# Kernel optimization log

Hardware: AMD Instinct MI355X
Metric: run time of the kernel (lower is better)

## Reference

```python
import jax, jax.numpy as jnp
import numpy as np

NUM_HEADS = 16

def setup_inputs() -> dict:
    key = jax.random.key(0)
    k1, k2, k3 = jax.random.split(key, 3)
    T, B, E = 2048, 4, 1024
    x = jax.random.normal(k1, (T, B, E), dtype=jnp.float32)
    # xavier-ish scale for weights
    in_proj_w = jax.random.normal(k2, (3 * E, E), dtype=jnp.float32) * (1.0 / np.sqrt(E))
    in_proj_b = jnp.zeros((3 * E,), dtype=jnp.float32)
    out_w = jax.random.normal(k3, (E, E), dtype=jnp.float32) * (1.0 / np.sqrt(E))
    out_b = jnp.zeros((E,), dtype=jnp.float32)
    return {"x": x, "in_proj_w": in_proj_w, "in_proj_b": in_proj_b, "out_w": out_w, "out_b": out_b}

def reference(x, in_proj_w, in_proj_b, out_w, out_b):
    # Self-attention (qkv_same path), dropout=0, eval mode, no masks.
    T, B, E = x.shape
    H = NUM_HEADS
    Dh = E // H
    scaling = Dh ** (-0.5)
    # fused in-projection: [T,B,3E]
    qkv = jnp.einsum('tbe,fe->tbf', x, in_proj_w) + in_proj_b
    q, k, v = jnp.split(qkv, 3, axis=-1)
    q = q * scaling
    # [T,B,E] -> [B,H,T,Dh]
    def to_heads(t):
        return t.reshape(T, B, H, Dh).transpose(1, 2, 0, 3)
    q, k, v = to_heads(q), to_heads(k), to_heads(v)
    # full TxT score matrix, softmax in float32 (matches F.softmax(..., dtype=float32))
    scores = jnp.einsum('bhtd,bhsd->bhts', q, k)
    attn_weights = jax.nn.softmax(scores.astype(jnp.float32), axis=-1).astype(scores.dtype)
    attn = jnp.einsum('bhts,bhsd->bhtd', attn_weights, v)
    # [B,H,T,Dh] -> [T,B,E]
    attn = attn.transpose(2, 0, 1, 3).reshape(T, B, E)
    attn = jnp.einsum('tbe,fe->tbf', attn, out_w) + out_b
    # need_weights=True: average over heads -> [B,T,T]
    avg_weights = attn_weights.sum(axis=1) / H
    return attn, avg_weights
```

## Files before the change

kernel.cpp:

```cpp
#include <hip/hip_runtime.h>
#include <stdint.h>

#define DEV __device__ __forceinline__

typedef __attribute__((ext_vector_type(8))) __bf16 bf16x8;
typedef __attribute__((ext_vector_type(4))) __bf16 bf16x4;
typedef __attribute__((ext_vector_type(4))) float f32x4;

DEV unsigned short f2bf(float f){
  union { float fv; unsigned u; } v; v.fv = f;
  unsigned r = v.u + 0x7fffu + ((v.u >> 16) & 1u);
  return (unsigned short)(r >> 16);
}

DEV void gload16(const void* g, void* l){
  __builtin_amdgcn_global_load_lds((const __attribute__((address_space(1))) void*)g,
                                   (__attribute__((address_space(3))) void*)l,
                                   16, 0, 0);
}

__global__ void k_cvt(const float* __restrict__ src, unsigned short* __restrict__ dst){
  const int i = (blockIdx.x * blockDim.x + threadIdx.x) << 2;
  const float4 v = *(const float4*)(src + i);
  ushort4 o;
  o.x = f2bf(v.x); o.y = f2bf(v.y); o.z = f2bf(v.z); o.w = f2bf(v.w);
  *(ushort4*)(dst + i) = o;
}

template<int MODE>
__launch_bounds__(256)
__global__ void k_gemm(const unsigned short* __restrict__ A,
                       const unsigned short* __restrict__ Bm,
                       const float* __restrict__ bias,
                       float* __restrict__ outF,
                       unsigned short* __restrict__ Qm,
                       unsigned short* __restrict__ Km,
                       unsigned short* __restrict__ VTm)
{
  __shared__ unsigned short As[128*64];
  __shared__ unsigned short Bs[128*64];
  const int tid  = threadIdx.x;
  const int lane = tid & 63;
  const int wid  = tid >> 6;
  const int wr   = wid >> 1;
  const int wc   = wid & 1;
  const int wg = blockIdx.x;
  int bx, by;
  if (MODE == 0){ const int slot = wg >> 3; bx = (wg & 7) + 8*(slot >> 6); by = slot & 63; }
  else          { bx = wg & 7; by = wg >> 3; }
  const int r0   = by * 128;
  const int c0   = bx * 128;
  const int l15  = lane & 15;
  const int l4   = lane >> 4;

  f32x4 acc[4][4];
#pragma unroll
  for (int m = 0; m < 4; ++m)
#pragma unroll
    for (int n = 0; n < 4; ++n)
      acc[m][n] = (f32x4){0.f, 0.f, 0.f, 0.f};

  for (int k0 = 0; k0 < 1024; k0 += 64){
#pragma unroll
    for (int i = 0; i < 4; ++i){
      const int sb   = (i*4 + wid)*64;
      const int slot = sb + lane;
      const int row  = slot >> 3;
      const int cg   = (slot & 7) ^ (row & 7);
      gload16(A  + (size_t)(r0 + row)*1024 + k0 + cg*8, (void*)(As + sb*8));
      gload16(Bm + (size_t)(c0 + row)*1024 + k0 + cg*8, (void*)(Bs + sb*8));
    }
    __syncthreads();
#pragma unroll
    for (int kk = 0; kk < 2; ++kk){
      bf16x8 af[4], bf[4];
#pragma unroll
      for (int m = 0; m < 4; ++m){
        const int row = wr*64 + m*16 + l15;
        const int ch  = (kk*4 + l4) ^ (row & 7);
        af[m] = *(const bf16x8*)(As + row*64 + ch*8);
      }
#pragma unroll
      for (int n = 0; n < 4; ++n){
        const int row = wc*64 + n*16 + l15;
        const int ch  = (kk*4 + l4) ^ (row & 7);
        bf[n] = *(const bf16x8*)(Bs + row*64 + ch*8);
      }
#pragma unroll
      for (int m = 0; m < 4; ++m)
#pragma unroll
        for (int n = 0; n < 4; ++n)
          acc[m][n] = __builtin_amdgcn_mfma_f32_16x16x32_bf16(af[m], bf[n], acc[m][n], 0, 0, 0);
    }
    __syncthreads();
  }

  if (MODE == 0){
#pragma unroll
    for (int n = 0; n < 4; ++n){
      const int f     = c0 + wc*64 + n*16 + l15;
      const float bs  = bias[f];
      const int which = f >> 10;
      const int fi    = f & 1023;
      const int h     = fi >> 6;
      const int d     = fi & 63;
#pragma unroll
      for (int m = 0; m < 4; ++m){
        const int rb = r0 + wr*64 + m*16 + (l4 << 2);
#pragma unroll
        for (int j = 0; j < 4; ++j){
          const int r = rb + j;
          const int t = r >> 2;
          const int b = r & 3;
          float v = acc[m][n][j] + bs;
          if (which == 0) v *= 0.18033688f;
          const unsigned short bv = f2bf(v);
          const int bh = b*16 + h;
          if (which == 0)      Qm [((size_t)bh*2048 + t)*64 + d] = bv;
          else if (which == 1) Km [((size_t)bh*2048 + t)*64 + d] = bv;
          else                 VTm[((size_t)bh*64 + d)*2048 + t] = bv;
        }
      }
    }
  } else {
#pragma unroll
    for (int m = 0; m < 4; ++m){
      const int rb = r0 + wr*64 + m*16 + (l4 << 2);
#pragma unroll
      for (int n = 0; n < 4; ++n){
        const int f    = c0 + wc*64 + n*16 + l15;
        const float bs = bias[f];
#pragma unroll
        for (int j = 0; j < 4; ++j)
          outF[(size_t)(rb + j)*1024 + f] = acc[m][n][j] + bs;
      }
    }
  }
}

__launch_bounds__(512)
__global__ void k_pv(const unsigned short* __restrict__ Qm,
                     const unsigned short* __restrict__ Km,
                     const unsigned short* __restrict__ VTm,
                     float* __restrict__ linv,
                     unsigned short* __restrict__ ctx)
{
  __shared__ unsigned short Ws[256*64];
  __shared__ unsigned short Ks[2][64*64];
  __shared__ unsigned short Vs[2][64*64];
  const int tid = threadIdx.x, lane = tid & 63, wid = tid >> 6;
  const int l15 = lane & 15, l4 = lane >> 4;
  const int wg = blockIdx.x;
  const int slot = wg >> 3;
  const int bh = (wg & 7)*8 + (slot >> 3);
  const int t0 = (slot & 7) * 256;
  const unsigned short* Qb = Qm  + (size_t)bh*131072;
  const unsigned short* Kb = Km  + (size_t)bh*131072;
  const unsigned short* Vb = VTm + (size_t)bh*131072;

  {
    const int s = tid;
    const int row = s >> 3;
    const int cg = (s & 7) ^ (row & 7);
    gload16(Kb + (size_t)row*64 + cg*8, (void*)(Ks[0] + s*8));
    gload16(Vb + (size_t)row*2048 + cg*8, (void*)(Vs[0] + s*8));
  }
  bf16x8 aq[2][2];
#pragma unroll
  for (int qs = 0; qs < 2; ++qs)
#pragma unroll
    for (int kk = 0; kk < 2; ++kk)
      aq[qs][kk] = *(const bf16x8*)(Qb + (size_t)(t0 + wid*32 + qs*16 + l15)*64 + (kk*4 + l4)*8);
  __syncthreads();

  f32x4 oacc[2][4];
#pragma unroll
  for (int qs = 0; qs < 2; ++qs)
#pragma unroll
    for (int n = 0; n < 4; ++n) oacc[qs][n] = (f32x4){0.f,0.f,0.f,0.f};
  float lacc[2] = {0.f, 0.f};
  const int rx = l15 & 7;

  for (int s0 = 0; s0 < 2048; s0 += 64){
    const int cur = (s0 >> 6) & 1;
    if (s0 + 64 < 2048){
      const int s = tid;
      const int row = s >> 3;
      const int cg = (s & 7) ^ (row & 7);
      gload16(Kb + (size_t)(s0 + 64 + row)*64 + cg*8, (void*)(Ks[cur^1] + s*8));
      gload16(Vb + (size_t)row*2048 + (s0 + 64) + cg*8, (void*)(Vs[cur^1] + s*8));
    }
#pragma unroll
    for (int n = 0; n < 4; ++n){
      bf16x8 ak[2];
#pragma unroll
      for (int kk = 0; kk < 2; ++kk){
        const int ch = (kk*4 + l4) ^ rx;
        ak[kk] = *(const bf16x8*)(Ks[cur] + (n*16 + l15)*64 + ch*8);
      }
#pragma unroll
      for (int qs = 0; qs < 2; ++qs){
        f32x4 sacc = (f32x4){0.f,0.f,0.f,0.f};
        sacc = __builtin_amdgcn_mfma_f32_16x16x32_bf16(ak[0], aq[qs][0], sacc, 0, 0, 0);
        sacc = __builtin_amdgcn_mfma_f32_16x16x32_bf16(ak[1], aq[qs][1], sacc, 0, 0, 0);
        f32x4 pv;
        pv[0] = __builtin_amdgcn_exp2f(sacc[0]);
        pv[1] = __builtin_amdgcn_exp2f(sacc[1]);
        pv[2] = __builtin_amdgcn_exp2f(sacc[2]);
        pv[3] = __builtin_amdgcn_exp2f(sacc[3]);
        lacc[qs] += (pv[0] + pv[1]) + (pv[2] + pv[3]);
        const bf16x4 pb = __builtin_convertvector(pv, bf16x4);
        const int wrow = wid*32 + qs*16 + l15;
        const int g = (n*4 + l4) ^ (rx << 1);
        *(bf16x4*)(Ws + wrow*64 + g*4) = pb;
      }
    }
    bf16x8 aw[2][2];
#pragma unroll
    for (int qs = 0; qs < 2; ++qs)
#pragma unroll
      for (int kk = 0; kk < 2; ++kk){
        const int c = (kk*4 + l4) ^ rx;
        aw[qs][kk] = *(const bf16x8*)(Ws + (wid*32 + qs*16 + l15)*64 + c*8);
      }
#pragma unroll
    for (int n = 0; n < 4; ++n){
#pragma unroll
      for (int kk = 0; kk < 2; ++kk){
        const int ch = (kk*4 + l4) ^ rx;
        const bf16x8 bv = *(const bf16x8*)(Vs[cur] + (n*16 + l15)*64 + ch*8);
#pragma unroll
        for (int qs = 0; qs < 2; ++qs)
          oacc[qs][n] = __builtin_amdgcn_mfma_f32_16x16x32_bf16(aw[qs][kk], bv, oacc[qs][n], 0, 0, 0);
      }
    }
    __syncthreads();
  }

  const int b = bh >> 4, h = bh & 15;
#pragma unroll
  for (int qs = 0; qs < 2; ++qs){
    lacc[qs] += __shfl_xor(lacc[qs], 16);
    lacc[qs] += __shfl_xor(lacc[qs], 32);
    const float rl = 1.0f / lacc[qs];
    if (lane < 16)
      linv[(size_t)bh*2048 + t0 + wid*32 + qs*16 + lane] = rl;
    float rlj[4];
#pragma unroll
    for (int j = 0; j < 4; ++j)
      rlj[j] = __shfl(rl, (l4 << 2) + j);
#pragma unroll
    for (int n = 0; n < 4; ++n){
#pragma unroll
      for (int j = 0; j < 4; ++j){
        const int t = t0 + wid*32 + qs*16 + (l4 << 2) + j;
        const int d = n*16 + l15;
        ctx[((size_t)t*4 + b)*1024 + h*64 + d] = f2bf(oacc[qs][n][j] * rlj[j]);
      }
    }
  }
}

__launch_bounds__(256)
__global__ void k_avg(const unsigned short* __restrict__ Qm,
                      const unsigned short* __restrict__ Km,
                      const float* __restrict__ linv,
                      float* __restrict__ avg)
{
  __shared__ unsigned short Ks[2][128*64];
  const int tid = threadIdx.x, lane = tid & 63, wid = tid >> 6;
  const int l15 = lane & 15, l4 = lane >> 4;
  const int wg = blockIdx.x;
  const int slot = wg >> 3;
  const int combo = (wg & 7) + 8*(slot >> 4);
  const int b   = combo >> 4;
  const int s0  = (combo & 15) * 128;
  const int t0  = (slot & 15) * 128;
  const int rx  = l15 & 7;

  float wacc[2][8][4];
#pragma unroll
  for (int qs = 0; qs < 2; ++qs)
#pragma unroll
    for (int n = 0; n < 8; ++n)
#pragma unroll
      for (int j = 0; j < 4; ++j) wacc[qs][n][j] = 0.f;

  {
    const unsigned short* Kb = Km + (size_t)(b*16)*131072;
#pragma unroll
    for (int i = 0; i < 4; ++i){
      const int s = i*256 + tid;
      const int row = s >> 3;
      const int cg = (s & 7) ^ (row & 7);
      gload16(Kb + (size_t)(s0 + row)*64 + cg*8, (void*)(Ks[0] + s*8));
    }
  }
  __syncthreads();

  for (int h = 0; h < 16; ++h){
    const int cur = h & 1;
    if (h < 15){
      const unsigned short* Kb = Km + (size_t)(b*16 + h + 1)*131072;
#pragma unroll
      for (int i = 0; i < 4; ++i){
        const int s = i*256 + tid;
        const int row = s >> 3;
        const int cg = (s & 7) ^ (row & 7);
        gload16(Kb + (size_t)(s0 + row)*64 + cg*8, (void*)(Ks[cur^1] + s*8));
      }
    }
    const int bh = b*16 + h;
    const unsigned short* Qb = Qm + (size_t)bh*131072;

    bf16x8 aq[2][2];
#pragma unroll
    for (int qs = 0; qs < 2; ++qs)
#pragma unroll
      for (int kk = 0; kk < 2; ++kk)
        aq[qs][kk] = *(const bf16x8*)(Qb + (size_t)(t0 + wid*32 + qs*16 + l15)*64 + (kk*4 + l4)*8);

    float4 lj[2];
#pragma unroll
    for (int qs = 0; qs < 2; ++qs){
      lj[qs] = *(const float4*)(linv + (size_t)bh*2048 + t0 + wid*32 + qs*16 + (l4 << 2));
      lj[qs].x *= 0.0625f; lj[qs].y *= 0.0625f; lj[qs].z *= 0.0625f; lj[qs].w *= 0.0625f;
    }

#pragma unroll
    for (int n = 0; n < 8; ++n){
      bf16x8 bk[2];
#pragma unroll
      for (int kk = 0; kk < 2; ++kk){
        const int ch = (kk*4 + l4) ^ rx;
        bk[kk] = *(const bf16x8*)(Ks[cur] + (n*16 + l15)*64 + ch*8);
      }
#pragma unroll
      for (int qs = 0; qs < 2; ++qs){
        f32x4 sacc = (f32x4){0.f,0.f,0.f,0.f};
        sacc = __builtin_amdgcn_mfma_f32_16x16x32_bf16(aq[qs][0], bk[0], sacc, 0, 0, 0);
        sacc = __builtin_amdgcn_mfma_f32_16x16x32_bf16(aq[qs][1], bk[1], sacc, 0, 0, 0);
        wacc[qs][n][0] += __builtin_amdgcn_exp2f(sacc[0]) * lj[qs].x;
        wacc[qs][n][1] += __builtin_amdgcn_exp2f(sacc[1]) * lj[qs].y;
        wacc[qs][n][2] += __builtin_amdgcn_exp2f(sacc[2]) * lj[qs].z;
        wacc[qs][n][3] += __builtin_amdgcn_exp2f(sacc[3]) * lj[qs].w;
      }
    }
    __syncthreads();
  }

#pragma unroll
  for (int qs = 0; qs < 2; ++qs)
#pragma unroll
    for (int n = 0; n < 8; ++n)
#pragma unroll
      for (int j = 0; j < 4; ++j){
        const int t = t0 + wid*32 + qs*16 + (l4 << 2) + j;
        const int s = s0 + n*16 + l15;
        avg[((size_t)b*2048 + t)*2048 + s] = wacc[qs][n][j];
      }
}

extern "C" void kernel_launch(void* const* d_in, const int* in_sizes, int n_in,
                              void* d_out, int out_size, void* d_ws, size_t ws_size,
                              hipStream_t stream)
{
  const float* x    = (const float*)d_in[0];
  const float* wqkv = (const float*)d_in[1];
  const float* bqkv = (const float*)d_in[2];
  const float* wout = (const float*)d_in[3];
  const float* bout = (const float*)d_in[4];
  float* out = (float*)d_out;

  char* ws = (char*)d_ws;
  unsigned short* xb    = (unsigned short*)(ws);
  unsigned short* wqkvb = (unsigned short*)(ws + ((size_t)16 << 20));
  unsigned short* woutb = (unsigned short*)(ws + ((size_t)24 << 20));
  unsigned short* Qm    = (unsigned short*)(ws + ((size_t)26 << 20));
  unsigned short* Km    = (unsigned short*)(ws + ((size_t)42 << 20));
  unsigned short* VTm   = (unsigned short*)(ws + ((size_t)58 << 20));
  unsigned short* ctx   = (unsigned short*)(ws + ((size_t)74 << 20));
  float* linv = (float*)(ws + ((size_t)90 << 20));

  k_cvt<<<8192, 256, 0, stream>>>(x,    xb);
  k_cvt<<<3072, 256, 0, stream>>>(wqkv, wqkvb);
  k_cvt<<<1024, 256, 0, stream>>>(wout, woutb);

  k_gemm<0><<<1536, 256, 0, stream>>>(xb, wqkvb, bqkv, nullptr, Qm, Km, VTm);
  k_pv     <<< 512, 512, 0, stream>>>(Qm, Km, VTm, linv, ctx);
  k_avg    <<<1024, 256, 0, stream>>>(Qm, Km, linv, out + 8388608);
  k_gemm<1><<< 512, 256, 0, stream>>>(ctx, woutb, bout, out, nullptr, nullptr, nullptr);
}
```

Before: 287.4 us.

## Double-buffer GEMM LDS tiles with 128x256 tiles and 512-thread blocks

Rewrites the projection GEMM kernel to use 512-thread blocks computing 128x256 output tiles, with double-buffered LDS so the next K-slice loads while MFMAs run on the current one. Raw s_waitcnt/s_barrier replaces __syncthreads, and s_setprio raises priority around the MFMA bursts. Block-to-tile mapping is changed to group row tiles for L2 reuse. The larger LDS footprint (96KB) and launch_bounds(512,1) limit occupancy to one block per CU, and the hand-written vmcnt count must match the number of outstanding loads.

```diff
diff --git a/kernel.cpp b/kernel.cpp
--- a/kernel.cpp
+++ b/kernel.cpp
@@ -28,7 +28,7 @@
 }
 
 template<int MODE>
-__launch_bounds__(256)
+__launch_bounds__(512, 1)
 __global__ void k_gemm(const unsigned short* __restrict__ A,
                        const unsigned short* __restrict__ Bm,
                        const float* __restrict__ bias,
@@ -37,21 +37,20 @@
                        unsigned short* __restrict__ Km,
                        unsigned short* __restrict__ VTm)
 {
-  __shared__ unsigned short As[128*64];
-  __shared__ unsigned short Bs[128*64];
+  __shared__ unsigned short As[2][128*64];
+  __shared__ unsigned short Bs[2][256*64];
   const int tid  = threadIdx.x;
   const int lane = tid & 63;
   const int wid  = tid >> 6;
-  const int wr   = wid >> 1;
-  const int wc   = wid & 1;
-  const int wg = blockIdx.x;
-  int bx, by;
-  if (MODE == 0){ const int slot = wg >> 3; bx = (wg & 7) + 8*(slot >> 6); by = slot & 63; }
-  else          { bx = wg & 7; by = wg >> 3; }
-  const int r0   = by * 128;
-  const int c0   = bx * 128;
+  const int wr   = wid >> 2;
+  const int wc   = wid & 3;
   const int l15  = lane & 15;
   const int l4   = lane >> 4;
+  const int wg  = blockIdx.x;
+  const int by  = (wg & 7)*8 + ((wg >> 3) & 7);
+  const int bx  = wg >> 6;
+  const int r0  = by * 128;
+  const int c0  = bx * 256;
 
   f32x4 acc[4][4];
 #pragma unroll
@@ -60,17 +59,25 @@
     for (int n = 0; n < 4; ++n)
       acc[m][n] = (f32x4){0.f, 0.f, 0.f, 0.f};
 
-  for (int k0 = 0; k0 < 1024; k0 += 64){
+  auto STAGE = [&](int buf, int kt){
+    const int k0 = kt << 6;
+#pragma unroll
+    for (int i = 0; i < 2; ++i){
+      const int s = i*512 + tid;
+      const int row = s >> 3;
+      const int cg = (s & 7) ^ (row & 7);
+      gload16(A + (size_t)(r0 + row)*1024 + k0 + cg*8, (void*)(&As[buf][s*8]));
+    }
 #pragma unroll
     for (int i = 0; i < 4; ++i){
-      const int sb   = (i*4 + wid)*64;
-      const int slot = sb + lane;
-      const int row  = slot >> 3;
-      const int cg   = (slot & 7) ^ (row & 7);
-      gload16(A  + (size_t)(r0 + row)*1024 + k0 + cg*8, (void*)(As + sb*8));
-      gload16(Bm + (size_t)(c0 + row)*1024 + k0 + cg*8, (void*)(Bs + sb*8));
-    }
-    __syncthreads();
+      const int s = i*512 + tid;
+      const int row = s >> 3;
+      const int cg = (s & 7) ^ (row & 7);
+      gload16(Bm + (size_t)(c0 + row)*1024 + k0 + cg*8, (void*)(&Bs[buf][s*8]));
+    }
+  };
+
+  auto COMPUTE = [&](int buf){
 #pragma unroll
     for (int kk = 0; kk < 2; ++kk){
       bf16x8 af[4], bf[4];
@@ -78,22 +85,36 @@
       for (int m = 0; m < 4; ++m){
         const int row = wr*64 + m*16 + l15;
         const int ch  = (kk*4 + l4) ^ (row & 7);
-        af[m] = *(const bf16x8*)(As + row*64 + ch*8);
+        af[m] = *(const bf16x8*)(&As[buf][row*64 + ch*8]);
       }
 #pragma unroll
       for (int n = 0; n < 4; ++n){
         const int row = wc*64 + n*16 + l15;
         const int ch  = (kk*4 + l4) ^ (row & 7);
-        bf[n] = *(const bf16x8*)(Bs + row*64 + ch*8);
-      }
+        bf[n] = *(const bf16x8*)(&Bs[buf][row*64 + ch*8]);
+      }
+      __builtin_amdgcn_s_setprio(1);
 #pragma unroll
       for (int m = 0; m < 4; ++m)
 #pragma unroll
         for (int n = 0; n < 4; ++n)
           acc[m][n] = __builtin_amdgcn_mfma_f32_16x16x32_bf16(af[m], bf[n], acc[m][n], 0, 0, 0);
-    }
-    __syncthreads();
-  }
+      __builtin_amdgcn_s_setprio(0);
+    }
+  };
+
+  STAGE(0, 0);
+  for (int t = 0; t < 15; ++t){
+    const int cur = t & 1;
+    STAGE(cur ^ 1, t + 1);
+    asm volatile("s_waitcnt vmcnt(6)" ::: "memory");
+    asm volatile("s_barrier" ::: "memory");
+    COMPUTE(cur);
+    asm volatile("s_barrier" ::: "memory");
+  }
+  asm volatile("s_waitcnt vmcnt(0)" ::: "memory");
+  asm volatile("s_barrier" ::: "memory");
+  COMPUTE(1);
 
   if (MODE == 0){
 #pragma unroll
@@ -386,8 +407,8 @@
   k_cvt<<<3072, 256, 0, stream>>>(wqkv, wqkvb);
   k_cvt<<<1024, 256, 0, stream>>>(wout, woutb);
 
-  k_gemm<0><<<1536, 256, 0, stream>>>(xb, wqkvb, bqkv, nullptr, Qm, Km, VTm);
-  k_pv     <<< 512, 512, 0, stream>>>(Qm, Km, VTm, linv, ctx);
+  k_gemm<0><<<768, 512, 0, stream>>>(xb, wqkvb, bqkv, nullptr, Qm, Km, VTm);
+  k_pv     <<<512, 512, 0, stream>>>(Qm, Km, VTm, linv, ctx);
   k_avg    <<<1024, 256, 0, stream>>>(Qm, Km, linv, out + 8388608);
-  k_gemm<1><<< 512, 256, 0, stream>>>(ctx, woutb, bout, out, nullptr, nullptr, nullptr);
-}
+  k_gemm<1><<<256, 512, 0, stream>>>(ctx, woutb, bout, out, nullptr, nullptr, nullptr);
+}
```

After: 282.1 us. No clear change (-1.9%).
